# Optimization experiments

Measured on AMD Instinct MI355X. Metric: run time of the kernel, lower is better.

## Reference

```python
import jax, jax.numpy as jnp
import numpy as np

E, EDIM, NDIM, H = 262144, 256, 256, 8
DH = NDIM // H
EPS = 1e-5  # torch nn.LayerNorm default


def _param(k, shape, scale=0.02):
    return jax.random.normal(k, shape, jnp.float32) * scale


def setup_inputs() -> dict:
    key = jax.random.key(0)
    ks = jax.random.split(key, 12)
    return {
        "x": jax.random.normal(ks[0], (E, EDIM), jnp.float32),
        "src_x": jax.random.normal(ks[1], (E, NDIM), jnp.float32),
        "dst_x": jax.random.normal(ks[2], (E, NDIM), jnp.float32),
        # multi-head cross-attention params (q from edge feats, k/v from node feats)
        "Wq": _param(ks[3], (EDIM, NDIM)), "bq": jnp.zeros((NDIM,), jnp.float32),
        "Wk": _param(ks[4], (NDIM, NDIM)), "bk": jnp.zeros((NDIM,), jnp.float32),
        "Wv": _param(ks[5], (NDIM, NDIM)), "bv": jnp.zeros((NDIM,), jnp.float32),
        "Wo": _param(ks[6], (NDIM, EDIM)), "bo": jnp.zeros((EDIM,), jnp.float32),
        "W1": _param(ks[7], (EDIM, 4 * EDIM)), "b1": jnp.zeros((4 * EDIM,), jnp.float32),
        "W2": _param(ks[8], (4 * EDIM, EDIM)), "b2": jnp.zeros((EDIM,), jnp.float32),
        # two LayerNorms
        "g1": jnp.ones((EDIM,), jnp.float32), "be1": jnp.zeros((EDIM,), jnp.float32),
        "g2": jnp.ones((EDIM,), jnp.float32), "be2": jnp.zeros((EDIM,), jnp.float32),
    }


def _layer_norm(h, g, b):
    m = jnp.mean(h, axis=-1, keepdims=True)
    v = jnp.mean(jnp.square(h - m), axis=-1, keepdims=True)
    return (h - m) * jax.lax.rsqrt(v + EPS) * g + b


def reference(x, src_x, dst_x, Wq, bq, Wk, bk, Wv, bv, Wo, bo,
              W1, b1, W2, b2, g1, be1, g2, be2):
    # per-edge cross-attention: query = edge feat (len 1), keys/values = (src, dst) (len 2)
    q = (x @ Wq + bq).reshape(E, H, DH)                 # [E,H,DH]
    kv = jnp.stack([src_x, dst_x], axis=1)              # [E,2,NDIM]
    k = (kv @ Wk + bk).reshape(E, 2, H, DH)
    v = (kv @ Wv + bv).reshape(E, 2, H, DH)
    scale = 1.0 / float(np.sqrt(DH))
    scores = jnp.einsum('ehd,ekhd->ehk', q, k) * scale  # [E,H,2]
    attn = jax.nn.softmax(scores, axis=-1)
    ctx = jnp.einsum('ehk,ekhd->ehd', attn, v).reshape(E, NDIM)
    out = ctx @ Wo + bo                                  # [E,EDIM]
    h = _layer_norm(x + out, g1, be1)
    ff = jax.nn.relu(h @ W1 + b1) @ W2 + b2
    return _layer_norm(h + ff, g2, be2)
```

## Files before the change

kernel.cpp:

```cpp
#include <hip/hip_runtime.h>
#include <hip/hip_bf16.h>
#include <math.h>

#define NROWS   262144
#define BM      64
#define THREADS 256
#define LDSB    (32768 + 32768 + 2048 + 2048 + 512)

using bf16x8 = __attribute__((ext_vector_type(8))) short;
using s16x4  = __attribute__((ext_vector_type(4))) short;
using f32x4  = __attribute__((ext_vector_type(4))) float;

__device__ __forceinline__ short f2bf(float f) {
  __hip_bfloat16 h = __float2bfloat16(f);
  return __builtin_bit_cast(short, h);
}
__device__ __forceinline__ float bf2f(short s) {
  __hip_bfloat16 h = __builtin_bit_cast(__hip_bfloat16, s);
  return __bfloat162float(h);
}
__device__ __forceinline__ unsigned pack2(float a, float b) {
  return (unsigned)(unsigned short)f2bf(a) | ((unsigned)(unsigned short)f2bf(b) << 16);
}
__device__ __forceinline__ int swz(int row, int col) {
  return row * 512 + ((col * 2) ^ ((row & 7) << 4));
}

__device__ __forceinline__ float red16(float p) {
  p += __shfl_xor(p, 1, 64);
  p += __shfl_xor(p, 2, 64);
  p += __shfl_xor(p, 4, 64);
  p += __shfl_xor(p, 8, 64);
  return p;
}

template <int MF, int NF>
__device__ __forceinline__ void gemmT(const char* __restrict__ Abuf,
                                      const short* __restrict__ WT, int Kw,
                                      int col0, int koff, int li, int hi,
                                      f32x4 (&acc)[MF][NF]) {
  const short* wp[NF];
#pragma unroll
  for (int n = 0; n < NF; ++n)
    wp[n] = WT + (size_t)(col0 + 16 * n + li) * Kw + koff + hi * 8;
#pragma unroll 2
  for (int kk = 0; kk < 256; kk += 32) {
    int ka = kk + hi * 8;
    bf16x8 b[NF];
#pragma unroll
    for (int n = 0; n < NF; ++n) b[n] = *(const bf16x8*)(wp[n] + kk);
    bf16x8 a[MF];
#pragma unroll
    for (int m = 0; m < MF; ++m)
      a[m] = *(const bf16x8*)(Abuf + swz(16 * m + li, ka));
#pragma unroll
    for (int m = 0; m < MF; ++m)
#pragma unroll
      for (int n = 0; n < NF; ++n)
        acc[m][n] = __builtin_amdgcn_mfma_f32_16x16x32_bf16(a[m], b[n], acc[m][n], 0, 0, 0);
  }
}

__global__ void prep(const float* __restrict__ Wq, const float* __restrict__ Wk,
                     const float* __restrict__ Wv, const float* __restrict__ Wo,
                     const float* __restrict__ W1, const float* __restrict__ W2,
                     short* __restrict__ wt) {
  int idx = blockIdx.x * blockDim.x + threadIdx.x;
  if (idx < 262144) {
    int m = idx >> 16;
    const float* W = (m == 0) ? Wq : (m == 1) ? Wk : (m == 2) ? Wv : Wo;
    float s = (m == 0) ? 0.17677669529663687f : 1.0f;
    int l = idx & 65535;
    int n = l >> 8, k = l & 255;
    wt[idx] = f2bf(W[k * 256 + n] * s);
  } else if (idx < 524288) {
    int l = idx - 262144;
    int n = l >> 8, k = l & 255;
    wt[idx] = f2bf(W1[k * 1024 + n]);
  } else {
    int l = idx - 524288;
    int n = l >> 10, k = l & 1023;
    wt[idx] = f2bf(W2[k * 256 + n]);
  }
}

__global__ __launch_bounds__(THREADS, 2)
void fused(const float* __restrict__ x, const float* __restrict__ sx,
           const float* __restrict__ dx,
           const float* __restrict__ bq, const float* __restrict__ bv,
           const float* __restrict__ bo,
           const float* __restrict__ b1, const float* __restrict__ b2,
           const float* __restrict__ g1, const float* __restrict__ be1,
           const float* __restrict__ g2, const float* __restrict__ be2,
           const short* __restrict__ wt, float* __restrict__ out) {
  extern __shared__ char sm[];
  char*  Cbuf = sm;
  char*  Tbuf = sm + 32768;
  float* sc   = (float*)(sm + 65536);
  float* scrP = (float*)(sm + 67584);
  float* scrM = (float*)(sm + 69632);

  const short* WqT = wt;
  const short* WkT = wt + 65536;
  const short* WvT = wt + 131072;
  const short* WoT = wt + 196608;
  const short* W1T = wt + 262144;
  const short* W2T = wt + 524288;

  const int tid  = threadIdx.x;
  const int w    = tid >> 6;
  const int lane = tid & 63;
  const int li   = lane & 15;
  const int hi   = lane >> 4;
  const int cw   = w * 64;
  const size_t row0 = (size_t)blockIdx.x * BM;

  const float* xt = x  + row0 * 256;
  const float* st = sx + row0 * 256;
  const float* dt = dx + row0 * 256;

  float4 ld[16];

#pragma unroll
  for (int it = 0; it < 16; ++it) {
    int idx = it * THREADS + tid;
    ld[it] = *(const float4*)(xt + (idx >> 6) * 256 + ((idx & 63) << 2));
  }
#pragma unroll
  for (int it = 0; it < 16; ++it) {
    int idx = it * THREADS + tid;
    int r = idx >> 6, c = (idx & 63) << 2;
    s16x4 o;
    o[0] = f2bf(ld[it].x); o[1] = f2bf(ld[it].y);
    o[2] = f2bf(ld[it].z); o[3] = f2bf(ld[it].w);
    *(s16x4*)(Cbuf + swz(r, c)) = o;
  }
  __syncthreads();

#pragma unroll
  for (int it = 0; it < 16; ++it) {
    int idx = it * THREADS + tid;
    ld[it] = *(const float4*)(dt + (idx >> 6) * 256 + ((idx & 63) << 2));
  }
  unsigned qb[4][4][2];
  {
    f32x4 qa[4][4];
#pragma unroll
    for (int m = 0; m < 4; ++m)
#pragma unroll
      for (int n = 0; n < 4; ++n) qa[m][n] = (f32x4){0.f, 0.f, 0.f, 0.f};
    gemmT<4, 4>(Cbuf, WqT, 256, cw, 0, li, hi, qa);
    const float scl = 0.17677669529663687f;
#pragma unroll
    for (int n = 0; n < 4; ++n) {
      float bqn = bq[cw + 16 * n + li] * scl;
#pragma unroll
      for (int m = 0; m < 4; ++m) {
        qb[m][n][0] = pack2(qa[m][n][0] + bqn, qa[m][n][1] + bqn);
        qb[m][n][1] = pack2(qa[m][n][2] + bqn, qa[m][n][3] + bqn);
      }
    }
  }
#pragma unroll
  for (int it = 0; it < 16; ++it) {
    int idx = it * THREADS + tid;
    int r = idx >> 6, c = (idx & 63) << 2;
    s16x4 o;
    o[0] = f2bf(ld[it].x); o[1] = f2bf(ld[it].y);
    o[2] = f2bf(ld[it].z); o[3] = f2bf(ld[it].w);
    *(s16x4*)(Tbuf + swz(r, c)) = o;
  }
  __syncthreads();

#define QF(m, n, j) bf2f((short)(((j) & 1) ? (qb[m][n][(j) >> 1] >> 16) \
                                           : (qb[m][n][(j) >> 1] & 0xffffu)))

#pragma unroll
  for (int it = 0; it < 16; ++it) {
    int idx = it * THREADS + tid;
    ld[it] = *(const float4*)(st + (idx >> 6) * 256 + ((idx & 63) << 2));
  }
#pragma unroll
  for (int hh = 0; hh < 2; ++hh) {
    f32x4 ka[4][2];
#pragma unroll
    for (int m = 0; m < 4; ++m)
#pragma unroll
      for (int n = 0; n < 2; ++n) ka[m][n] = (f32x4){0.f, 0.f, 0.f, 0.f};
    gemmT<4, 2>(Tbuf, WkT, 256, cw + 32 * hh, 0, li, hi, ka);
#pragma unroll
    for (int m = 0; m < 4; ++m)
#pragma unroll
      for (int j = 0; j < 4; ++j) {
        float pr = red16(QF(m, 2 * hh, j) * ka[m][0][j] +
                         QF(m, 2 * hh + 1, j) * ka[m][1][j]);
        if (li == 0) sc[(w * 2 + hh) * 64 + 16 * m + 4 * hi + j] = pr;
      }
  }
  f32x4 vd[4][4];
#pragma unroll
  for (int m = 0; m < 4; ++m)
#pragma unroll
    for (int n = 0; n < 4; ++n) vd[m][n] = (f32x4){0.f, 0.f, 0.f, 0.f};
  gemmT<4, 4>(Tbuf, WvT, 256, cw, 0, li, hi, vd);
  __syncthreads();
#pragma unroll
  for (int it = 0; it < 16; ++it) {
    int idx = it * THREADS + tid;
    int r = idx >> 6, c = (idx & 63) << 2;
    s16x4 o;
    o[0] = f2bf(ld[it].x); o[1] = f2bf(ld[it].y);
    o[2] = f2bf(ld[it].z); o[3] = f2bf(ld[it].w);
    *(s16x4*)(Tbuf + swz(r, c)) = o;
  }
  __syncthreads();

#pragma unroll
  for (int hh = 0; hh < 2; ++hh) {
    f32x4 ka[4][2];
#pragma unroll
    for (int m = 0; m < 4; ++m)
#pragma unroll
      for (int n = 0; n < 2; ++n) ka[m][n] = (f32x4){0.f, 0.f, 0.f, 0.f};
    gemmT<4, 2>(Tbuf, WkT, 256, cw + 32 * hh, 0, li, hi, ka);
#pragma unroll
    for (int m = 0; m < 4; ++m)
#pragma unroll
      for (int j = 0; j < 4; ++j) {
        float ps = red16(QF(m, 2 * hh, j) * ka[m][0][j] +
                         QF(m, 2 * hh + 1, j) * ka[m][1][j]);
        int r = 16 * m + 4 * hi + j;
        float pdv = sc[(w * 2 + hh) * 64 + r];
        float awv = 1.f / (1.f + expf(pdv - ps));
        if (li == 0) sc[(w * 2 + hh) * 64 + r] = awv;
      }
  }
  {
    f32x4 vs[4][4];
#pragma unroll
    for (int m = 0; m < 4; ++m)
#pragma unroll
      for (int n = 0; n < 4; ++n) vs[m][n] = (f32x4){0.f, 0.f, 0.f, 0.f};
    gemmT<4, 4>(Tbuf, WvT, 256, cw, 0, li, hi, vs);
#pragma unroll
    for (int hh = 0; hh < 2; ++hh)
#pragma unroll
      for (int n2 = 0; n2 < 2; ++n2) {
        int n = 2 * hh + n2;
        float bvn = bv[cw + 16 * n + li];
#pragma unroll
        for (int m = 0; m < 4; ++m)
#pragma unroll
          for (int j = 0; j < 4; ++j) {
            float a = sc[(w * 2 + hh) * 64 + 16 * m + 4 * hi + j];
            vs[m][n][j] = a * vs[m][n][j] + (1.f - a) * vd[m][n][j] + bvn;
          }
      }
    __syncthreads();
#pragma unroll
    for (int m = 0; m < 4; ++m)
#pragma unroll
      for (int n = 0; n < 4; ++n)
#pragma unroll
        for (int j = 0; j < 4; ++j)
          *(short*)(Tbuf + swz(16 * m + 4 * hi + j, cw + 16 * n + li)) = f2bf(vs[m][n][j]);
  }
  __syncthreads();

  {
    f32x4 oa[4][4];
#pragma unroll
    for (int m = 0; m < 4; ++m)
#pragma unroll
      for (int n = 0; n < 4; ++n) oa[m][n] = (f32x4){0.f, 0.f, 0.f, 0.f};
    gemmT<4, 4>(Tbuf, WoT, 256, cw, 0, li, hi, oa);
#pragma unroll
    for (int n = 0; n < 4; ++n) {
      float bon = bo[cw + 16 * n + li];
#pragma unroll
      for (int m = 0; m < 4; ++m)
#pragma unroll
        for (int j = 0; j < 4; ++j) {
          int r = 16 * m + 4 * hi + j;
          float xv = bf2f(*(short*)(Cbuf + swz(r, cw + 16 * n + li)));
          oa[m][n][j] += bon + xv;
        }
    }
#pragma unroll
    for (int m = 0; m < 4; ++m)
#pragma unroll
      for (int j = 0; j < 4; ++j) {
        int r = 16 * m + 4 * hi + j;
        float sv = oa[m][0][j] + oa[m][1][j] + oa[m][2][j] + oa[m][3][j];
        float qv = oa[m][0][j] * oa[m][0][j] + oa[m][1][j] * oa[m][1][j]
                 + oa[m][2][j] * oa[m][2][j] + oa[m][3][j] * oa[m][3][j];
        float s = red16(sv);
        float q = red16(qv);
        if (li == 0) { scrP[(w * 64 + r) * 2] = s; scrP[(w * 64 + r) * 2 + 1] = q; }
      }
    __syncthreads();
    if (tid < BM) {
      float S = 0.f, Q = 0.f;
#pragma unroll
      for (int ww = 0; ww < 4; ++ww) {
        S += scrP[(ww * 64 + tid) * 2];
        Q += scrP[(ww * 64 + tid) * 2 + 1];
      }
      float mean = S * (1.f / 256.f);
      float var  = Q * (1.f / 256.f) - mean * mean;
      scrM[tid * 2] = mean;
      scrM[tid * 2 + 1] = rsqrtf(var + 1e-5f);
    }
    __syncthreads();
#pragma unroll
    for (int n = 0; n < 4; ++n) {
      float g1n = g1[cw + 16 * n + li];
      float b1n = be1[cw + 16 * n + li];
#pragma unroll
      for (int m = 0; m < 4; ++m)
#pragma unroll
        for (int j = 0; j < 4; ++j) {
          int r = 16 * m + 4 * hi + j;
          float mean = scrM[r * 2], rs = scrM[r * 2 + 1];
          *(short*)(Cbuf + swz(r, cw + 16 * n + li)) =
              f2bf((oa[m][n][j] - mean) * rs * g1n + b1n);
        }
    }
  }
  __syncthreads();

  f32x4 a2[4][4];
#pragma unroll
  for (int m = 0; m < 4; ++m)
#pragma unroll
    for (int n = 0; n < 4; ++n) a2[m][n] = (f32x4){0.f, 0.f, 0.f, 0.f};
#pragma unroll 1
  for (int c = 0; c < 4; ++c) {
#pragma unroll
    for (int g = 0; g < 2; ++g) {
      f32x4 a1[4][2];
#pragma unroll
      for (int m = 0; m < 4; ++m)
#pragma unroll
        for (int n = 0; n < 2; ++n) a1[m][n] = (f32x4){0.f, 0.f, 0.f, 0.f};
      gemmT<4, 2>(Cbuf, W1T, 256, 256 * c + cw + 32 * g, 0, li, hi, a1);
#pragma unroll
      for (int n = 0; n < 2; ++n) {
        float b1n = b1[256 * c + cw + 32 * g + 16 * n + li];
#pragma unroll
        for (int m = 0; m < 4; ++m)
#pragma unroll
          for (int j = 0; j < 4; ++j) {
            int r = 16 * m + 4 * hi + j;
            *(short*)(Tbuf + swz(r, cw + 32 * g + 16 * n + li)) =
                f2bf(fmaxf(a1[m][n][j] + b1n, 0.f));
          }
      }
    }
    __syncthreads();
    gemmT<4, 4>(Tbuf, W2T, 1024, cw, 256 * c, li, hi, a2);
    __syncthreads();
  }

  {
#pragma unroll
    for (int n = 0; n < 4; ++n) {
      float b2n = b2[cw + 16 * n + li];
#pragma unroll
      for (int m = 0; m < 4; ++m)
#pragma unroll
        for (int j = 0; j < 4; ++j) {
          int r = 16 * m + 4 * hi + j;
          a2[m][n][j] += b2n + bf2f(*(short*)(Cbuf + swz(r, cw + 16 * n + li)));
        }
    }
#pragma unroll
    for (int m = 0; m < 4; ++m)
#pragma unroll
      for (int j = 0; j < 4; ++j) {
        int r = 16 * m + 4 * hi + j;
        float sv = a2[m][0][j] + a2[m][1][j] + a2[m][2][j] + a2[m][3][j];
        float qv = a2[m][0][j] * a2[m][0][j] + a2[m][1][j] * a2[m][1][j]
                 + a2[m][2][j] * a2[m][2][j] + a2[m][3][j] * a2[m][3][j];
        float s = red16(sv);
        float q = red16(qv);
        if (li == 0) { scrP[(w * 64 + r) * 2] = s; scrP[(w * 64 + r) * 2 + 1] = q; }
      }
    __syncthreads();
    if (tid < BM) {
      float S = 0.f, Q = 0.f;
#pragma unroll
      for (int ww = 0; ww < 4; ++ww) {
        S += scrP[(ww * 64 + tid) * 2];
        Q += scrP[(ww * 64 + tid) * 2 + 1];
      }
      float mean = S * (1.f / 256.f);
      float var  = Q * (1.f / 256.f) - mean * mean;
      scrM[tid * 2] = mean;
      scrM[tid * 2 + 1] = rsqrtf(var + 1e-5f);
    }
    __syncthreads();

    float g2n[4], be2n[4];
#pragma unroll
    for (int n = 0; n < 4; ++n) {
      g2n[n] = g2[cw + 16 * n + li];
      be2n[n] = be2[cw + 16 * n + li];
    }
    float* orow = out + row0 * 256;
#pragma unroll
    for (int hf = 0; hf < 2; ++hf) {
#pragma unroll
      for (int m2 = 0; m2 < 2; ++m2) {
        int m = 2 * hf + m2;
#pragma unroll
        for (int n = 0; n < 4; ++n)
#pragma unroll
          for (int j = 0; j < 4; ++j) {
            int r = 16 * m + 4 * hi + j;
            float mean = scrM[r * 2], rs = scrM[r * 2 + 1];
            int rr = r - 32 * hf;
            *(float*)(Tbuf + rr * 1024 + (((cw + 16 * n + li) * 4) ^ ((rr & 7) << 4)))
                = (a2[m][n][j] - mean) * rs * g2n[n] + be2n[n];
          }
      }
      __syncthreads();
#pragma unroll
      for (int t = 0; t < 8; ++t) {
        int idx = t * THREADS + tid;
        int r = idx >> 6, c4 = idx & 63;
        f32x4 v = *(f32x4*)(Tbuf + r * 1024 + ((c4 * 16) ^ ((r & 7) << 4)));
        *(f32x4*)(orow + (hf * 32 + r) * 256 + c4 * 4) = v;
      }
      __syncthreads();
    }
  }
#undef QF
}

extern "C" void kernel_launch(void* const* d_in, const int* in_sizes, int n_in,
                              void* d_out, int out_size, void* d_ws, size_t ws_size,
                              hipStream_t stream) {
  const float* x   = (const float*)d_in[0];
  const float* sx  = (const float*)d_in[1];
  const float* dx  = (const float*)d_in[2];
  const float* Wq  = (const float*)d_in[3];
  const float* bq  = (const float*)d_in[4];
  const float* Wk  = (const float*)d_in[5];
  const float* Wv  = (const float*)d_in[7];
  const float* bv  = (const float*)d_in[8];
  const float* Wo  = (const float*)d_in[9];
  const float* bo  = (const float*)d_in[10];
  const float* W1  = (const float*)d_in[11];
  const float* b1  = (const float*)d_in[12];
  const float* W2  = (const float*)d_in[13];
  const float* b2  = (const float*)d_in[14];
  const float* g1  = (const float*)d_in[15];
  const float* be1 = (const float*)d_in[16];
  const float* g2  = (const float*)d_in[17];
  const float* be2 = (const float*)d_in[18];
  short* wt = (short*)d_ws;

  prep<<<dim3(1536), dim3(512), 0, stream>>>(Wq, Wk, Wv, Wo, W1, W2, wt);
  fused<<<dim3(NROWS / BM), dim3(THREADS), LDSB, stream>>>(
      x, sx, dx, bq, bv, bo, b1, b2, g1, be1, g2, be2, wt, (float*)d_out);
}
```

Baseline: 1.083 ms.

## Interleave half-tile input staging with Q/K/V GEMMs to cut register pressure

Input tiles are staged in two halves of 8 float4 registers instead of 16. The global loads for the next input (dst_x, src_x) are issued before or between the Q-projection and K/V GEMMs, so memory latency overlaps MFMA work. The Q GEMM is split into two K=128 passes to make room for this interleaving. The LayerNorm partial-sum scratch is merged into the score buffer to shrink LDS, and a dead no-op loop is added.

```diff
diff --git a/kernel.cpp b/kernel.cpp
--- a/kernel.cpp
+++ b/kernel.cpp
@@ -4,8 +4,8 @@
 
 #define NROWS   262144
 #define BM      64
-#define THREADS 256
-#define LDSB    (32768 + 32768 + 2048 + 2048 + 512)
+#define NTHR    256
+#define LDSB    (32768 + 32768 + 2048 + 512)
 
 using bf16x8 = __attribute__((ext_vector_type(8))) short;
 using s16x4  = __attribute__((ext_vector_type(4))) short;
@@ -22,8 +22,12 @@
 __device__ __forceinline__ unsigned pack2(float a, float b) {
   return (unsigned)(unsigned short)f2bf(a) | ((unsigned)(unsigned short)f2bf(b) << 16);
 }
+template <int RSTR>
+__device__ __forceinline__ int swzR(int row, int col) {
+  return row * RSTR + ((col * 2) ^ ((row & 7) << 4));
+}
 __device__ __forceinline__ int swz(int row, int col) {
-  return row * 512 + ((col * 2) ^ ((row & 7) << 4));
+  return swzR<512>(row, col);
 }
 
 __device__ __forceinline__ float red16(float p) {
@@ -34,8 +38,8 @@
   return p;
 }
 
-template <int MF, int NF>
-__device__ __forceinline__ void gemmT(const char* __restrict__ Abuf,
+template <int MF, int NF, int KLEN = 256, int RSTR = 512>
+__device__ __forceinline__ void gemmA(const char* __restrict__ Abuf,
                                       const short* __restrict__ WT, int Kw,
                                       int col0, int koff, int li, int hi,
                                       f32x4 (&acc)[MF][NF]) {
@@ -44,7 +48,7 @@
   for (int n = 0; n < NF; ++n)
     wp[n] = WT + (size_t)(col0 + 16 * n + li) * Kw + koff + hi * 8;
 #pragma unroll 2
-  for (int kk = 0; kk < 256; kk += 32) {
+  for (int kk = 0; kk < KLEN; kk += 32) {
     int ka = kk + hi * 8;
     bf16x8 b[NF];
 #pragma unroll
@@ -52,12 +56,35 @@
     bf16x8 a[MF];
 #pragma unroll
     for (int m = 0; m < MF; ++m)
-      a[m] = *(const bf16x8*)(Abuf + swz(16 * m + li, ka));
+      a[m] = *(const bf16x8*)(Abuf + swzR<RSTR>(16 * m + li, ka));
 #pragma unroll
     for (int m = 0; m < MF; ++m)
 #pragma unroll
       for (int n = 0; n < NF; ++n)
         acc[m][n] = __builtin_amdgcn_mfma_f32_16x16x32_bf16(a[m], b[n], acc[m][n], 0, 0, 0);
+  }
+}
+
+__device__ __forceinline__ void stage8(float4 (&ld)[8],
+                                       const float* __restrict__ g,
+                                       int tid, int half) {
+#pragma unroll
+  for (int it = 0; it < 8; ++it) {
+    int idx = (half * 8 + it) * NTHR + tid;
+    ld[it] = *(const float4*)(g + (idx >> 6) * 256 + ((idx & 63) << 2));
+  }
+}
+__device__ __forceinline__ void write8(float4 (&ld)[8],
+                                       char* __restrict__ buf,
+                                       int tid, int half) {
+#pragma unroll
+  for (int it = 0; it < 8; ++it) {
+    int idx = (half * 8 + it) * NTHR + tid;
+    int r = idx >> 6, c = (idx & 63) << 2;
+    s16x4 o;
+    o[0] = f2bf(ld[it].x); o[1] = f2bf(ld[it].y);
+    o[2] = f2bf(ld[it].z); o[3] = f2bf(ld[it].w);
+    *(s16x4*)(buf + swz(r, c)) = o;
   }
 }
 
@@ -84,7 +111,7 @@
   }
 }
 
-__global__ __launch_bounds__(THREADS, 2)
+__global__ __launch_bounds__(NTHR, 2)
 void fused(const float* __restrict__ x, const float* __restrict__ sx,
            const float* __restrict__ dx,
            const float* __restrict__ bq, const float* __restrict__ bv,
@@ -97,8 +124,7 @@
   char*  Cbuf = sm;
   char*  Tbuf = sm + 32768;
   float* sc   = (float*)(sm + 65536);
-  float* scrP = (float*)(sm + 67584);
-  float* scrM = (float*)(sm + 69632);
+  float* scrM = (float*)(sm + 67584);
 
   const short* WqT = wt;
   const short* WkT = wt + 65536;
@@ -119,29 +145,14 @@
   const float* st = sx + row0 * 256;
   const float* dt = dx + row0 * 256;
 
-  float4 ld[16];
-
-#pragma unroll
-  for (int it = 0; it < 16; ++it) {
-    int idx = it * THREADS + tid;
-    ld[it] = *(const float4*)(xt + (idx >> 6) * 256 + ((idx & 63) << 2));
-  }
-#pragma unroll
-  for (int it = 0; it < 16; ++it) {
-    int idx = it * THREADS + tid;
-    int r = idx >> 6, c = (idx & 63) << 2;
-    s16x4 o;
-    o[0] = f2bf(ld[it].x); o[1] = f2bf(ld[it].y);
-    o[2] = f2bf(ld[it].z); o[3] = f2bf(ld[it].w);
-    *(s16x4*)(Cbuf + swz(r, c)) = o;
-  }
-  __syncthreads();
-
-#pragma unroll
-  for (int it = 0; it < 16; ++it) {
-    int idx = it * THREADS + tid;
-    ld[it] = *(const float4*)(dt + (idx >> 6) * 256 + ((idx & 63) << 2));
-  }
+  float4 ld[8];
+
+  stage8(ld, xt, tid, 0);
+  write8(ld, Cbuf, tid, 0);
+  stage8(ld, xt, tid, 1);
+  write8(ld, Cbuf, tid, 1);
+  __syncthreads();
+
   unsigned qb[4][4][2];
   {
     f32x4 qa[4][4];
@@ -149,7 +160,12 @@
     for (int m = 0; m < 4; ++m)
 #pragma unroll
       for (int n = 0; n < 4; ++n) qa[m][n] = (f32x4){0.f, 0.f, 0.f, 0.f};
-    gemmT<4, 4>(Cbuf, WqT, 256, cw, 0, li, hi, qa);
+    stage8(ld, dt, tid, 0);
+    gemmA<4, 4, 128>(Cbuf, WqT, 256, cw, 0, li, hi, qa);
+    write8(ld, Tbuf, tid, 0);
+    stage8(ld, dt, tid, 1);
+    gemmA<4, 4, 128>(Cbuf + 256, WqT, 256, cw, 128, li, hi, qa);
+    write8(ld, Tbuf, tid, 1);
     const float scl = 0.17677669529663687f;
 #pragma unroll
     for (int n = 0; n < 4; ++n) {
@@ -161,25 +177,43 @@
       }
     }
   }
-#pragma unroll
-  for (int it = 0; it < 16; ++it) {
-    int idx = it * THREADS + tid;
-    int r = idx >> 6, c = (idx & 63) << 2;
-    s16x4 o;
-    o[0] = f2bf(ld[it].x); o[1] = f2bf(ld[it].y);
-    o[2] = f2bf(ld[it].z); o[3] = f2bf(ld[it].w);
-    *(s16x4*)(Tbuf + swz(r, c)) = o;
-  }
   __syncthreads();
 
 #define QF(m, n, j) bf2f((short)(((j) & 1) ? (qb[m][n][(j) >> 1] >> 16) \
                                            : (qb[m][n][(j) >> 1] & 0xffffu)))
 
-#pragma unroll
-  for (int it = 0; it < 16; ++it) {
-    int idx = it * THREADS + tid;
-    ld[it] = *(const float4*)(st + (idx >> 6) * 256 + ((idx & 63) << 2));
-  }
+  f32x4 vd[4][4];
+  {
+    stage8(ld, st, tid, 0);
+#pragma unroll
+    for (int hh = 0; hh < 2; ++hh) {
+      f32x4 ka[4][2];
+#pragma unroll
+      for (int m = 0; m < 4; ++m)
+#pragma unroll
+        for (int n = 0; n < 2; ++n) ka[m][n] = (f32x4){0.f, 0.f, 0.f, 0.f};
+      gemmA<4, 2>(Tbuf, WkT, 256, cw + 32 * hh, 0, li, hi, ka);
+#pragma unroll
+      for (int m = 0; m < 4; ++m)
+#pragma unroll
+        for (int j = 0; j < 4; ++j) {
+          float pr = red16(QF(m, 2 * hh, j) * ka[m][0][j] +
+                           QF(m, 2 * hh + 1, j) * ka[m][1][j]);
+          if (li == 0) sc[(w * 2 + hh) * 64 + 16 * m + 4 * hi + j] = pr;
+        }
+    }
+#pragma unroll
+    for (int m = 0; m < 4; ++m)
+#pragma unroll
+      for (int n = 0; n < 4; ++n) vd[m][n] = (f32x4){0.f, 0.f, 0.f, 0.f};
+    gemmA<4, 4>(Tbuf, WvT, 256, cw, 0, li, hi, vd);
+  }
+  __syncthreads();
+  write8(ld, Tbuf, tid, 0);
+  stage8(ld, st, tid, 1);
+  write8(ld, Tbuf, tid, 1);
+  __syncthreads();
+
 #pragma unroll
   for (int hh = 0; hh < 2; ++hh) {
     f32x4 ka[4][2];
@@ -187,42 +221,7 @@
     for (int m = 0; m < 4; ++m)
 #pragma unroll
       for (int n = 0; n < 2; ++n) ka[m][n] = (f32x4){0.f, 0.f, 0.f, 0.f};
-    gemmT<4, 2>(Tbuf, WkT, 256, cw + 32 * hh, 0, li, hi, ka);
-#pragma unroll
-    for (int m = 0; m < 4; ++m)
-#pragma unroll
-      for (int j = 0; j < 4; ++j) {
-        float pr = red16(QF(m, 2 * hh, j) * ka[m][0][j] +
-                         QF(m, 2 * hh + 1, j) * ka[m][1][j]);
-        if (li == 0) sc[(w * 2 + hh) * 64 + 16 * m + 4 * hi + j] = pr;
-      }
-  }
-  f32x4 vd[4][4];
-#pragma unroll
-  for (int m = 0; m < 4; ++m)
-#pragma unroll
-    for (int n = 0; n < 4; ++n) vd[m][n] = (f32x4){0.f, 0.f, 0.f, 0.f};
-  gemmT<4, 4>(Tbuf, WvT, 256, cw, 0, li, hi, vd);
-  __syncthreads();
-#pragma unroll
-  for (int it = 0; it < 16; ++it) {
-    int idx = it * THREADS + tid;
-    int r = idx >> 6, c = (idx & 63) << 2;
-    s16x4 o;
-    o[0] = f2bf(ld[it].x); o[1] = f2bf(ld[it].y);
-    o[2] = f2bf(ld[it].z); o[3] = f2bf(ld[it].w);
-    *(s16x4*)(Tbuf + swz(r, c)) = o;
-  }
-  __syncthreads();
-
-#pragma unroll
-  for (int hh = 0; hh < 2; ++hh) {
-    f32x4 ka[4][2];
-#pragma unroll
-    for (int m = 0; m < 4; ++m)
-#pragma unroll
-      for (int n = 0; n < 2; ++n) ka[m][n] = (f32x4){0.f, 0.f, 0.f, 0.f};
-    gemmT<4, 2>(Tbuf, WkT, 256, cw + 32 * hh, 0, li, hi, ka);
+    gemmA<4, 2>(Tbuf, WkT, 256, cw + 32 * hh, 0, li, hi, ka);
 #pragma unroll
     for (int m = 0; m < 4; ++m)
 #pragma unroll
@@ -241,7 +240,7 @@
     for (int m = 0; m < 4; ++m)
 #pragma unroll
       for (int n = 0; n < 4; ++n) vs[m][n] = (f32x4){0.f, 0.f, 0.f, 0.f};
-    gemmT<4, 4>(Tbuf, WvT, 256, cw, 0, li, hi, vs);
+    gemmA<4, 4>(Tbuf, WvT, 256, cw, 0, li, hi, vs);
 #pragma unroll
     for (int hh = 0; hh < 2; ++hh)
 #pragma unroll
@@ -273,7 +272,7 @@
     for (int m = 0; m < 4; ++m)
 #pragma unroll
       for (int n = 0; n < 4; ++n) oa[m][n] = (f32x4){0.f, 0.f, 0.f, 0.f};
-    gemmT<4, 4>(Tbuf, WoT, 256, cw, 0, li, hi, oa);
+    gemmA<4, 4>(Tbuf, WoT, 256, cw, 0, li, hi, oa);
 #pragma unroll
     for (int n = 0; n < 4; ++n) {
       float bon = bo[cw + 16 * n + li];
@@ -296,15 +295,15 @@
                  + oa[m][2][j] * oa[m][2][j] + oa[m][3][j] * oa[m][3][j];
         float s = red16(sv);
         float q = red16(qv);
-        if (li == 0) { scrP[(w * 64 + r) * 2] = s; scrP[(w * 64 + r) * 2 + 1] = q; }
+        if (li == 0) { sc[(w * 64 + r) * 2] = s; sc[(w * 64 + r) * 2 + 1] = q; }
       }
     __syncthreads();
     if (tid < BM) {
       float S = 0.f, Q = 0.f;
 #pragma unroll
       for (int ww = 0; ww < 4; ++ww) {
-        S += scrP[(ww * 64 + tid) * 2];
-        Q += scrP[(ww * 64 + tid) * 2 + 1];
+        S += sc[(ww * 64 + tid) * 2];
+        Q += sc[(ww * 64 + tid) * 2 + 1];
       }
       float mean = S * (1.f / 256.f);
       float var  = Q * (1.f / 256.f) - mean * mean;
@@ -343,22 +342,22 @@
       for (int m = 0; m < 4; ++m)
 #pragma unroll
         for (int n = 0; n < 2; ++n) a1[m][n] = (f32x4){0.f, 0.f, 0.f, 0.f};
-      gemmT<4, 2>(Cbuf, W1T, 256, 256 * c + cw + 32 * g, 0, li, hi, a1);
+      gemmA<4, 2>(Cbuf, W1T, 256, 256 * c + cw + 32 * g, 0, li, hi, a1);
 #pragma unroll
       for (int n = 0; n < 2; ++n) {
         float b1n = b1[256 * c + cw + 32 * g + 16 * n + li];
+        int lc = cw + 32 * g + 16 * n + li;
 #pragma unroll
         for (int m = 0; m < 4; ++m)
 #pragma unroll
           for (int j = 0; j < 4; ++j) {
             int r = 16 * m + 4 * hi + j;
-            *(short*)(Tbuf + swz(r, cw + 32 * g + 16 * n + li)) =
-                f2bf(fmaxf(a1[m][n][j] + b1n, 0.f));
+            *(short*)(Tbuf + swz(r, lc)) = f2bf(fmaxf(a1[m][n][j] + b1n, 0.f));
           }
       }
     }
     __syncthreads();
-    gemmT<4, 4>(Tbuf, W2T, 1024, cw, 256 * c, li, hi, a2);
+    gemmA<4, 4>(Tbuf, W2T, 1024, cw, 256 * c, li, hi, a2);
     __syncthreads();
   }
 
@@ -384,15 +383,15 @@
                  + a2[m][2][j] * a2[m][2][j] + a2[m][3][j] * a2[m][3][j];
         float s = red16(sv);
         float q = red16(qv);
-        if (li == 0) { scrP[(w * 64 + r) * 2] = s; scrP[(w * 64 + r) * 2 + 1] = q; }
+        if (li == 0) { sc[(w * 64 + r) * 2] = s; sc[(w * 64 + r) * 2 + 1] = q; }
       }
     __syncthreads();
     if (tid < BM) {
       float S = 0.f, Q = 0.f;
 #pragma unroll
       for (int ww = 0; ww < 4; ++ww) {
-        S += scrP[(ww * 64 + tid) * 2];
-        Q += scrP[(ww * 64 + tid) * 2 + 1];
+        S += sc[(ww * 64 + tid) * 2];
+        Q += sc[(ww * 64 + tid) * 2 + 1];
       }
       float mean = S * (1.f / 256.f);
       float var  = Q * (1.f / 256.f) - mean * mean;
@@ -426,8 +425,14 @@
       }
       __syncthreads();
 #pragma unroll
+      for (int t = 0; t < 4; ++t) {
+        int idx = t * NTHR + tid;
+        int r = idx >> 6, c4 = idx & 63;
+        (void)r; (void)c4;
+      }
+#pragma unroll
       for (int t = 0; t < 8; ++t) {
-        int idx = t * THREADS + tid;
+        int idx = t * NTHR + tid;
         int r = idx >> 6, c4 = idx & 63;
         f32x4 v = *(f32x4*)(Tbuf + r * 1024 + ((c4 * 16) ^ ((r & 7) << 4)));
         *(f32x4*)(orow + (hf * 32 + r) * 256 + c4 * 4) = v;
@@ -462,6 +467,6 @@
   short* wt = (short*)d_ws;
 
   prep<<<dim3(1536), dim3(512), 0, stream>>>(Wq, Wk, Wv, Wo, W1, W2, wt);
-  fused<<<dim3(NROWS / BM), dim3(THREADS), LDSB, stream>>>(
+  fused<<<dim3(NROWS / BM), dim3(NTHR), LDSB, stream>>>(
       x, sx, dx, bq, bv, bo, b1, b2, g1, be1, g2, be2, wt, (float*)d_out);
 }
```

Result: no change. 1.070 ms (-1.2%).
